# Performance work log

Hardware: AMD Instinct MI355X
Metric: run time of the kernel (lower is better)

Reference implementation:

```python
import jax, jax.numpy as jnp
import numpy as np

MODEL_DIM = 1024
HEAD_SIZE = 128

def setup_inputs() -> dict:
    key = jax.random.key(0)
    k0, k1, k2, k3 = jax.random.split(key, 4)
    embedded = jax.random.normal(k0, (4, 4096, MODEL_DIM), dtype=jnp.float32)
    # nn.Linear(model_dim, head_size, bias=False) weights: [head_size, model_dim]
    s = 1.0 / np.sqrt(MODEL_DIM)
    Wk = jax.random.uniform(k1, (HEAD_SIZE, MODEL_DIM), jnp.float32, -s, s)
    Wq = jax.random.uniform(k2, (HEAD_SIZE, MODEL_DIM), jnp.float32, -s, s)
    Wv = jax.random.uniform(k3, (HEAD_SIZE, MODEL_DIM), jnp.float32, -s, s)
    return {"embedded": embedded, "Wk": Wk, "Wq": Wq, "Wv": Wv}

def reference(embedded, Wk, Wq, Wv):
    # embedded: [b, s, m]; W*: [h, m]
    keys = jnp.einsum('bsm,hm->bsh', embedded, Wk)
    queries = jnp.einsum('bsm,hm->bsh', embedded, Wq)
    values = jnp.einsum('bsm,hm->bsh', embedded, Wv)
    h = keys.shape[-1]
    scores = jnp.einsum('bqh,bkh->bqk', queries, keys) / jnp.sqrt(jnp.float32(h))  # [b,s,s]
    s_len = keys.shape[1]
    causal = jnp.tril(jnp.ones((s_len, s_len), dtype=bool))
    scores = jnp.where(causal, scores, -jnp.inf)
    probs = jax.nn.softmax(scores, axis=-1)
    return jnp.einsum('bqk,bkh->bqh', probs, values)
```

## Files before the change

kernel.cpp:

```cpp
#include <hip/hip_runtime.h>
#include <hip/hip_bf16.h>


#define SEQ 4096
#define BATCH 4
#define HS 128
#define SLOTS_PB 128

typedef unsigned short u16;
typedef __bf16 bf16x8 __attribute__((ext_vector_type(8)));
typedef _Float16 f16x4 __attribute__((ext_vector_type(4)));
typedef float f32x4 __attribute__((ext_vector_type(4)));

__device__ __forceinline__ u16 f2bf(float f) {
    union { float f; unsigned u; } v; v.f = f;
    unsigned u = v.u;
    return (u16)((u + 0x7FFFu + ((u >> 16) & 1u)) >> 16);
}
__device__ __forceinline__ float bf2f(u16 u) {
    union { unsigned u; float f; } v; v.u = ((unsigned)u) << 16; return v.f;
}
__device__ __forceinline__ u16 f2h(float f) {
    union { _Float16 h; u16 u; } v; v.h = (_Float16)f; return v.u;
}
__device__ __forceinline__ void async_cp16(const void* g, void* l) {
    __builtin_amdgcn_global_load_lds(
        (const __attribute__((address_space(1))) unsigned int*)g,
        (__attribute__((address_space(3))) unsigned int*)l, 16, 0, 0);
}
__device__ __forceinline__ int nsplit_of(int Q) {
    return Q / 5 + 1 + (Q >= 23 ? 1 : 0);
}

__global__ __launch_bounds__(256) void wconv_kernel(
    const float* __restrict__ Wk, const float* __restrict__ Wq,
    const float* __restrict__ Wv, u16* __restrict__ Wt)
{
    const int g    = blockIdx.x * 256 + threadIdx.x;
    const int lane = g & 63;
    const int kf   = (g >> 6) & 1;
    const int kc   = (g >> 7) & 15;
    const int nt   = g >> 11;
    const int row  = nt * 16 + (lane & 15);
    const int k0   = kc * 64 + kf * 32 + (lane >> 4) * 8;
    const float* src = (row < 128) ? Wk : ((row < 256) ? Wq : Wv);
    const float scale = (row >= 128 && row < 256)
        ? 0.08838834764831845f * 1.4426950408889634f : 1.0f;
    const float4 v0 = *(const float4*)&src[(size_t)(row & 127) * 1024 + k0];
    const float4 v1 = *(const float4*)&src[(size_t)(row & 127) * 1024 + k0 + 4];
    ushort4 a, b;
    a.x = f2bf(v0.x * scale); a.y = f2bf(v0.y * scale);
    a.z = f2bf(v0.z * scale); a.w = f2bf(v0.w * scale);
    b.x = f2bf(v1.x * scale); b.y = f2bf(v1.y * scale);
    b.z = f2bf(v1.z * scale); b.w = f2bf(v1.w * scale);
    *(ushort4*)&Wt[(size_t)g * 8]     = a;
    *(ushort4*)&Wt[(size_t)g * 8 + 4] = b;
}

__global__ __launch_bounds__(512, 4) void qkv_kernel(
    const float* __restrict__ emb, const u16* __restrict__ Wt,
    u16* __restrict__ Qf, u16* __restrict__ Kf, u16* __restrict__ Vf)
{
    __shared__ u16 sE[2][32][72];
    __shared__ u16 sOut[32][392];

    const int tid  = threadIdx.x;
    const int wv   = tid >> 6;
    const int lane = tid & 63;
    const int quad = lane >> 4;
    const int l16  = lane & 15;
    const int R0   = blockIdx.x * 32;

    const int arow = tid >> 4, ac4 = tid & 15;
    const float* abase = &emb[(size_t)(R0 + arow) * 1024 + ac4 * 4];

    f32x4 acc[2][3];
    #pragma unroll
    for (int rg = 0; rg < 2; rg++)
        #pragma unroll
        for (int j = 0; j < 3; j++) acc[rg][j] = (f32x4){0.f, 0.f, 0.f, 0.f};

    bf16x8 B0[6], B1[6];

#define LOADA(c) (*(const float4*)&abase[(size_t)(c) * 64])
#define LOADB(kci, B)                                                          \
    {                                                                          \
        _Pragma("unroll")                                                      \
        for (int j = 0; j < 3; j++) {                                          \
            const size_t g = ((size_t)((wv * 3 + j) * 16 + (kci)) * 2) * 64 + lane; \
            B[2 * j]     = *(const bf16x8*)&Wt[g * 8];                         \
            B[2 * j + 1] = *(const bf16x8*)&Wt[(g + 64) * 8];                  \
        }                                                                      \
    }
#define WRITEA(buf, v)                                                         \
    {                                                                          \
        ushort4 o;                                                             \
        o.x = f2bf((v).x); o.y = f2bf((v).y);                                  \
        o.z = f2bf((v).z); o.w = f2bf((v).w);                                  \
        *(ushort4*)&sE[buf][arow][ac4 * 4] = o;                                \
    }
#define COMPUTE(buf, B)                                                        \
    {                                                                          \
        bf16x8 a[2][2];                                                        \
        _Pragma("unroll")                                                      \
        for (int rg = 0; rg < 2; rg++)                                         \
            _Pragma("unroll")                                                  \
            for (int kf = 0; kf < 2; kf++)                                     \
                a[rg][kf] = *(const bf16x8*)&sE[buf][rg * 16 + l16][kf * 32 + quad * 8]; \
        _Pragma("unroll")                                                      \
        for (int j = 0; j < 3; j++)                                            \
            _Pragma("unroll")                                                  \
            for (int rg = 0; rg < 2; rg++) {                                   \
                acc[rg][j] = __builtin_amdgcn_mfma_f32_16x16x32_bf16(a[rg][0], B[2 * j],     acc[rg][j], 0, 0, 0); \
                acc[rg][j] = __builtin_amdgcn_mfma_f32_16x16x32_bf16(a[rg][1], B[2 * j + 1], acc[rg][j], 0, 0, 0); \
            }                                                                  \
    }

    float4 av = LOADA(0);
    LOADB(0, B0);
    WRITEA(0, av);

    for (int it = 0; it < 8; it++) {
        const int k1 = 2 * it + 1;
        __syncthreads();
        av = LOADA(k1);
        LOADB(k1, B1);
        COMPUTE(0, B0);
        WRITEA(1, av);
        __syncthreads();
        if (it < 7) {
            av = LOADA(k1 + 1);
            LOADB(k1 + 1, B0);
        }
        COMPUTE(1, B1);
        if (it < 7) WRITEA(0, av);
    }

    #pragma unroll
    for (int j = 0; j < 3; j++) {
        const int col = wv * 48 + j * 16 + l16;
        #pragma unroll
        for (int rg = 0; rg < 2; rg++) {
            const int rl = rg * 16 + quad * 4;
            #pragma unroll
            for (int r = 0; r < 4; r++) {
                const float v = acc[rg][j][r];
                sOut[rl + r][col] = (col < 256) ? f2bf(v) : f2h(v);
            }
        }
    }
    __syncthreads();

    const int b  = R0 >> 12;
    const int s0 = R0 & 4095;
    {
        const int g    = tid;
        const int lg   = g & 63;
        const int kfp  = (g >> 6) & 3;
        const int k16l = g >> 8;
        const int rl   = k16l * 16 + (lg & 15);
        const int cl   = kfp * 32 + (lg >> 4) * 8;
        const size_t base = (((size_t)(b * 256 + (s0 >> 4) + k16l) * 4 + kfp) * 64 + lg) * 8;
        *(uint4*)&Kf[base] = *(const uint4*)&sOut[rl][cl];
        *(uint4*)&Qf[base] = *(const uint4*)&sOut[rl][128 + cl];
    }
    #pragma unroll
    for (int i = 0; i < 2; i++) {
        const int g   = tid + i * 512;
        const int lg  = g & 63;
        const int ntl = (g >> 6) & 1;
        const int ht  = g >> 7;
        const int h   = ht * 16 + (lg & 15);
        const int kl  = ntl * 16 + ((lg >> 4) & 3) * 4;
        ushort4 o;
        o.x = sOut[kl + 0][256 + h];
        o.y = sOut[kl + 1][256 + h];
        o.z = sOut[kl + 2][256 + h];
        o.w = sOut[kl + 3][256 + h];
        const int t64 = s0 >> 6;
        const int ntg = ((s0 >> 4) & 3) + ntl;
        const size_t base = ((((size_t)(b * 64 + t64) * 8 + ht) * 4 + ntg) * 64 + lg) * 4;
        *(ushort4*)&Vf[base] = o;
    }
#undef LOADA
#undef LOADB
#undef WRITEA
#undef COMPUTE
}

template<bool DIRECT>
__global__ __launch_bounds__(512, 4) void attn_kernel(
    const u16* __restrict__ Qf, const u16* __restrict__ Kf,
    const u16* __restrict__ Vf, u16* __restrict__ Opart,
    float* __restrict__ lpart, float* __restrict__ out)
{
    __shared__ u16 sT[3][8192];

    const int tid  = threadIdx.x;
    const int wv   = tid >> 6;
    const int lane = tid & 63;
    const int quad = lane >> 4;
    const int l16  = lane & 15;

    const int L    = blockIdx.x;
    const int b    = L & 3;
    const int slot = L >> 2;

    int Q = 0, sp = 0;
    if constexpr (DIRECT) {
        Q = slot; sp = 0;
    } else {
        int acc = 0;
        #pragma unroll 1
        for (int qq = 0; qq < 32; ++qq) {
            const int n = nsplit_of(qq);
            if (slot < acc + n) { Q = qq; sp = slot - acc; break; }
            acc += n;
        }
    }
    const int total = 4 * Q + 4;
    const int ns    = DIRECT ? 1 : nsplit_of(Q);
    const int kbeg  = DIRECT ? 0 : (sp * total) / ns;
    const int kend  = DIRECT ? total : ((sp + 1) * total) / ns;

    const int q0 = Q * 128;
    const size_t bS = (size_t)b * SEQ;

    const char* KbB = (const char*)(Kf + (size_t)b * 524288);
    const char* VbB = (const char*)(Vf + (size_t)b * 524288);

    bf16x8 qf[4];
    const int q16 = Q * 8 + wv;
    #pragma unroll
    for (int kf = 0; kf < 4; kf++)
        qf[kf] = *(const bf16x8*)&Qf[(((size_t)(b * 256 + q16) * 4 + kf) * 64 + lane) * 8];

    float rs0 = 0.f;
    f32x4 O[8];
    #pragma unroll
    for (int ht = 0; ht < 8; ht++) O[ht] = (f32x4){0.f, 0.f, 0.f, 0.f};

    const int qg0 = q0 + wv * 16 + l16;

#define STAGE(bufi, kt)                                                        \
    {                                                                          \
        async_cp16(KbB + (size_t)(kt) * 8192 + wv * 1024 + lane * 16,          \
                   (char*)&sT[bufi][0] + wv * 1024);                           \
        async_cp16(VbB + ((((size_t)((kt) >> 1) * 8 + wv) * 4 + ((kt) & 1) * 2) << 9) + lane * 16, \
                   (char*)&sT[bufi][4096] + wv * 1024);                        \
    }
#define WAITBAR(N)                                                             \
    {                                                                          \
        asm volatile("s_waitcnt vmcnt(" #N ")" ::: "memory");                  \
        __builtin_amdgcn_sched_barrier(0);                                     \
        __builtin_amdgcn_s_barrier();                                          \
        __builtin_amdgcn_sched_barrier(0);                                     \
    }

    STAGE(0, kbeg);
    STAGE(1, kbeg + 1);
    WAITBAR(2);

    int bcur = 0;
    for (int kt = kbeg; kt < kend; ++kt) {
        const bool more = (kt + 2 < kend);
        if (more) {
            const int b2 = (bcur >= 1) ? bcur - 1 : bcur + 2;
            STAGE(b2, kt + 2);
        }

        const bool diag = (kt >= 4 * Q);
        f16x4 pf0[2];
        #pragma unroll
        for (int nt = 0; nt < 2; nt++) {
            f32x4 s0 = (f32x4){0.f, 0.f, 0.f, 0.f};
            __builtin_amdgcn_s_setprio(1);
            #pragma unroll
            for (int kf = 0; kf < 4; kf++) {
                const bf16x8 kfr = *(const bf16x8*)&sT[bcur][((nt * 4 + kf) << 9) + lane * 8];
                s0 = __builtin_amdgcn_mfma_f32_16x16x32_bf16(kfr, qf[kf], s0, 0, 0, 0);
            }
            __builtin_amdgcn_s_setprio(0);
            if (diag) {
                #pragma unroll
                for (int r = 0; r < 4; r++) {
                    const int kg = kt * 32 + nt * 16 + quad * 4 + r;
                    if (kg > qg0) s0[r] = -3.0e38f;
                }
            }
            f16x4 p0;
            #pragma unroll
            for (int r = 0; r < 4; r++) {
                const float e0 = exp2f(s0[r] - 4.0f);
                rs0 += e0;
                p0[r] = (_Float16)e0;
            }
            pf0[nt] = p0;
        }

        __builtin_amdgcn_s_setprio(1);
        #pragma unroll
        for (int ht = 0; ht < 8; ht++) {
            f16x4 vf[2];
            #pragma unroll
            for (int nt = 0; nt < 2; nt++)
                vf[nt] = *(const f16x4*)&sT[bcur][4096 + ((ht * 2 + nt) << 8) + lane * 4];
            #pragma unroll
            for (int nt = 0; nt < 2; nt++)
                O[ht] = __builtin_amdgcn_mfma_f32_16x16x16f16(vf[nt], pf0[nt], O[ht], 0, 0, 0);
        }
        __builtin_amdgcn_s_setprio(0);

        if (more) { WAITBAR(2); } else { WAITBAR(0); }
        bcur = (bcur == 2) ? 0 : bcur + 1;
    }
#undef STAGE
#undef WAITBAR

    rs0 += __shfl_xor(rs0, 16); rs0 += __shfl_xor(rs0, 32);

    if constexpr (DIRECT) {
        const float inv = 1.0f / rs0;
        const int q = q0 + wv * 16 + l16;
        #pragma unroll
        for (int ht = 0; ht < 8; ht++) {
            f32x4 o = O[ht] * inv;
            *(f32x4*)&out[(bS + q) * HS + ht * 16 + quad * 4] = o;
        }
    } else {
        const size_t slotbase = (size_t)b * SLOTS_PB + slot;
        #pragma unroll
        for (int ht = 0; ht < 8; ht++) {
            const size_t j = ((slotbase * 8 + wv) * 8 + ht) * 64 + lane;
            ushort4 o;
            o.x = f2bf(O[ht][0]); o.y = f2bf(O[ht][1]);
            o.z = f2bf(O[ht][2]); o.w = f2bf(O[ht][3]);
            *(ushort4*)&Opart[j * 4] = o;
        }
        if (quad == 0)
            lpart[slotbase * 128 + wv * 16 + l16] = rs0;
    }
}

__global__ __launch_bounds__(256) void merge_kernel(
    const u16* __restrict__ Opart, const float* __restrict__ lpart,
    float* __restrict__ out)
{
    const int g    = blockIdx.x * 256 + threadIdx.x;
    const int lane = g & 63;
    const int ht   = (g >> 6) & 7;
    const int wvv  = (g >> 9) & 7;
    const int Q    = (g >> 12) & 31;
    const int b    = g >> 17;
    const int l16  = lane & 15;
    const int qd   = lane >> 4;

    int pre = 0, ns = 0;
    #pragma unroll 1
    for (int qq = 0; qq < 32; ++qq) {
        const int n = nsplit_of(qq);
        if (qq < Q) pre += n;
        else if (qq == Q) { ns = n; break; }
    }
    const size_t base_slot = (size_t)b * SLOTS_PB + pre;
    const int ql = wvv * 16 + l16;

    float den = 0.f;
    f32x4 num = (f32x4){0.f, 0.f, 0.f, 0.f};
    #pragma unroll 1
    for (int s = 0; s < ns; s++) {
        den += lpart[(base_slot + s) * 128 + ql];
        const size_t j = (((base_slot + s) * 8 + wvv) * 8 + ht) * 64 + lane;
        const ushort4 o = *(const ushort4*)&Opart[j * 4];
        num[0] += bf2f(o.x); num[1] += bf2f(o.y);
        num[2] += bf2f(o.z); num[3] += bf2f(o.w);
    }
    const float inv = 1.0f / den;
    float4 o; o.x = num[0] * inv; o.y = num[1] * inv;
    o.z = num[2] * inv; o.w = num[3] * inv;
    const size_t off = ((size_t)b << 19) +
                       (size_t)(Q * 128 + wvv * 16 + l16) * 128 +
                       (size_t)(ht * 4 + qd) * 4;
    *(float4*)&out[off] = o;
}

extern "C" void kernel_launch(void* const* d_in, const int* in_sizes, int n_in,
                              void* d_out, int out_size, void* d_ws, size_t ws_size,
                              hipStream_t stream) {
    const float* emb = (const float*)d_in[0];
    const float* Wk  = (const float*)d_in[1];
    const float* Wq  = (const float*)d_in[2];
    const float* Wv  = (const float*)d_in[3];
    float* out = (float*)d_out;

    char* ws = (char*)d_ws;
    const size_t WBF_SZ    = (size_t)384 * 1024 * 2;
    const size_t QKV_SZ    = (size_t)BATCH * SEQ * HS * 2;
    const size_t Q_OFF     = WBF_SZ;
    const size_t K_OFF     = Q_OFF + QKV_SZ;
    const size_t V_OFF     = K_OFF + QKV_SZ;
    const size_t OPART_OFF = V_OFF + QKV_SZ;
    const size_t OPART_SZ  = (size_t)BATCH * SLOTS_PB * 32768;
    const size_t L_SZ      = (size_t)BATCH * SLOTS_PB * 128 * 4;

    u16* Wt = (u16*)ws;
    u16* Qf = (u16*)(ws + Q_OFF);
    u16* Kf = (u16*)(ws + K_OFF);
    u16* Vf = (u16*)(ws + V_OFF);

    wconv_kernel<<<dim3(192), dim3(256), 0, stream>>>(Wk, Wq, Wv, Wt);
    qkv_kernel<<<dim3(512), dim3(512), 0, stream>>>(emb, Wt, Qf, Kf, Vf);

    const size_t need = OPART_OFF + OPART_SZ + L_SZ;

    if (ws_size >= need) {
        u16*   Opart = (u16*)(ws + OPART_OFF);
        float* lp    = (float*)(ws + OPART_OFF + OPART_SZ);
        attn_kernel<false><<<dim3(4 * SLOTS_PB), dim3(512), 0, stream>>>(Qf, Kf, Vf, Opart, lp, out);
        merge_kernel<<<dim3(BATCH * SEQ * HS / 4 / 256), dim3(256), 0, stream>>>(Opart, lp, out);
    } else {
        attn_kernel<true><<<dim3(32 * BATCH), dim3(512), 0, stream>>>(Qf, Kf, Vf, nullptr, nullptr, out);
    }
}
```

Before: 163.8 us.

## Stage full 32x1024 embedding tile in LDS upfront for QKV projection

The QKV kernel now loads the whole 32-row embedding slab (converted to bf16) into shared memory once at the start, instead of double-buffering 64-column chunks with two barriers per iteration. The main K loop then runs with only weight prefetches and no __syncthreads. The output staging buffer is unioned with the slab to limit LDS use. The cost is about 66KB of LDS per block, which likely cuts occupancy below the launch_bounds target. Global loads of the slab are also no longer overlapped with MFMA work.

```diff
diff --git a/kernel.cpp b/kernel.cpp
--- a/kernel.cpp
+++ b/kernel.cpp
@@ -61,8 +61,10 @@
     const float* __restrict__ emb, const u16* __restrict__ Wt,
     u16* __restrict__ Qf, u16* __restrict__ Kf, u16* __restrict__ Vf)
 {
-    __shared__ u16 sE[2][32][72];
-    __shared__ u16 sOut[32][392];
+    __shared__ union {
+        u16 sE[32][1032];
+        u16 sOut[32][392];
+    } sm;
 
     const int tid  = threadIdx.x;
     const int wv   = tid >> 6;
@@ -71,8 +73,21 @@
     const int l16  = lane & 15;
     const int R0   = blockIdx.x * 32;
 
-    const int arow = tid >> 4, ac4 = tid & 15;
-    const float* abase = &emb[(size_t)(R0 + arow) * 1024 + ac4 * 4];
+    {
+        const float4* srcA = (const float4*)&emb[(size_t)R0 * 1024];
+        #pragma unroll 4
+        for (int i = 0; i < 16; i++) {
+            const int f   = i * 512 + tid;
+            const float4 v = srcA[f];
+            const int row = f >> 8;
+            const int c4  = f & 255;
+            ushort4 o;
+            o.x = f2bf(v.x); o.y = f2bf(v.y);
+            o.z = f2bf(v.z); o.w = f2bf(v.w);
+            *(ushort4*)&sm.sE[row][c4 * 4] = o;
+        }
+    }
+    __syncthreads();
 
     f32x4 acc[2][3];
     #pragma unroll
@@ -82,7 +97,6 @@
 
     bf16x8 B0[6], B1[6];
 
-#define LOADA(c) (*(const float4*)&abase[(size_t)(c) * 64])
 #define LOADB(kci, B)                                                          \
     {                                                                          \
         _Pragma("unroll")                                                      \
@@ -92,21 +106,14 @@
             B[2 * j + 1] = *(const bf16x8*)&Wt[(g + 64) * 8];                  \
         }                                                                      \
     }
-#define WRITEA(buf, v)                                                         \
-    {                                                                          \
-        ushort4 o;                                                             \
-        o.x = f2bf((v).x); o.y = f2bf((v).y);                                  \
-        o.z = f2bf((v).z); o.w = f2bf((v).w);                                  \
-        *(ushort4*)&sE[buf][arow][ac4 * 4] = o;                                \
-    }
-#define COMPUTE(buf, B)                                                        \
+#define COMPUTE(c, B)                                                          \
     {                                                                          \
         bf16x8 a[2][2];                                                        \
         _Pragma("unroll")                                                      \
         for (int rg = 0; rg < 2; rg++)                                         \
             _Pragma("unroll")                                                  \
             for (int kf = 0; kf < 2; kf++)                                     \
-                a[rg][kf] = *(const bf16x8*)&sE[buf][rg * 16 + l16][kf * 32 + quad * 8]; \
+                a[rg][kf] = *(const bf16x8*)&sm.sE[rg * 16 + l16][(c) * 64 + kf * 32 + quad * 8]; \
         _Pragma("unroll")                                                      \
         for (int j = 0; j < 3; j++)                                            \
             _Pragma("unroll")                                                  \
@@ -116,25 +123,14 @@
             }                                                                  \
     }
 
-    float4 av = LOADA(0);
     LOADB(0, B0);
-    WRITEA(0, av);
-
     for (int it = 0; it < 8; it++) {
-        const int k1 = 2 * it + 1;
-        __syncthreads();
-        av = LOADA(k1);
-        LOADB(k1, B1);
-        COMPUTE(0, B0);
-        WRITEA(1, av);
-        __syncthreads();
-        if (it < 7) {
-            av = LOADA(k1 + 1);
-            LOADB(k1 + 1, B0);
-        }
-        COMPUTE(1, B1);
-        if (it < 7) WRITEA(0, av);
-    }
+        LOADB(2 * it + 1, B1);
+        COMPUTE(2 * it, B0);
+        if (it < 7) LOADB(2 * it + 2, B0);
+        COMPUTE(2 * it + 1, B1);
+    }
+    __syncthreads();
 
     #pragma unroll
     for (int j = 0; j < 3; j++) {
@@ -145,7 +141,7 @@
             #pragma unroll
             for (int r = 0; r < 4; r++) {
                 const float v = acc[rg][j][r];
-                sOut[rl + r][col] = (col < 256) ? f2bf(v) : f2h(v);
+                sm.sOut[rl + r][col] = (col < 256) ? f2bf(v) : f2h(v);
             }
         }
     }
@@ -161,8 +157,8 @@
         const int rl   = k16l * 16 + (lg & 15);
         const int cl   = kfp * 32 + (lg >> 4) * 8;
         const size_t base = (((size_t)(b * 256 + (s0 >> 4) + k16l) * 4 + kfp) * 64 + lg) * 8;
-        *(uint4*)&Kf[base] = *(const uint4*)&sOut[rl][cl];
-        *(uint4*)&Qf[base] = *(const uint4*)&sOut[rl][128 + cl];
+        *(uint4*)&Kf[base] = *(const uint4*)&sm.sOut[rl][cl];
+        *(uint4*)&Qf[base] = *(const uint4*)&sm.sOut[rl][128 + cl];
     }
     #pragma unroll
     for (int i = 0; i < 2; i++) {
@@ -173,18 +169,16 @@
         const int h   = ht * 16 + (lg & 15);
         const int kl  = ntl * 16 + ((lg >> 4) & 3) * 4;
         ushort4 o;
-        o.x = sOut[kl + 0][256 + h];
-        o.y = sOut[kl + 1][256 + h];
-        o.z = sOut[kl + 2][256 + h];
-        o.w = sOut[kl + 3][256 + h];
+        o.x = sm.sOut[kl + 0][256 + h];
+        o.y = sm.sOut[kl + 1][256 + h];
+        o.z = sm.sOut[kl + 2][256 + h];
+        o.w = sm.sOut[kl + 3][256 + h];
         const int t64 = s0 >> 6;
         const int ntg = ((s0 >> 4) & 3) + ntl;
         const size_t base = ((((size_t)(b * 64 + t64) * 8 + ht) * 4 + ntg) * 64 + lg) * 4;
         *(ushort4*)&Vf[base] = o;
     }
-#undef LOADA
 #undef LOADB
-#undef WRITEA
 #undef COMPUTE
 }
 
```

After: 154.5 us (median of 2 runs). 1.06x faster.
